# Optimization experiments

Measured on AMD Instinct MI355X. Metric: run time of the kernel, lower is better.

The kernel has to match this reference:

```python
import jax, jax.numpy as jnp
import numpy as np

HID = 128

def setup_inputs() -> dict:
    key = jax.random.key(0)
    ks = jax.random.split(key, 16)
    T, N, E = 32, 10000, 160000
    features = jax.random.normal(ks[0], (T, N, 1), dtype=jnp.float32)
    src = jax.random.randint(ks[1], (E,), 0, N)
    dst = jax.random.randint(ks[2], (E,), 0, N)
    s = 0.1
    # GraphConv params (stored as [in,out] so y = x @ W + b)
    W1 = jax.random.normal(ks[3], (1, 32), dtype=jnp.float32) * s
    b1 = jnp.zeros((32,), jnp.float32)
    W2 = jax.random.normal(ks[4], (32, HID), dtype=jnp.float32) * s
    b2 = jnp.zeros((HID,), jnp.float32)
    # attention-pool gate nn.Linear(128,1)
    gate_w = jax.random.normal(ks[5], (HID, 1), dtype=jnp.float32) * s
    gate_b = jnp.zeros((1,), jnp.float32)
    # GRU params, PyTorch layout: [3H, in], gate order (r, z, n)
    W_ih = jax.random.normal(ks[6], (3 * HID, HID), dtype=jnp.float32) * s
    W_hh = jax.random.normal(ks[7], (3 * HID, HID), dtype=jnp.float32) * s
    b_ih = jnp.zeros((3 * HID,), jnp.float32)
    b_hh = jnp.zeros((3 * HID,), jnp.float32)
    # dense layers ([in,out])
    d1_w = jax.random.normal(ks[8], (HID, 16), dtype=jnp.float32) * s
    d1_b = jnp.zeros((16,), jnp.float32)
    d2_w = jax.random.normal(ks[9], (16, 4), dtype=jnp.float32) * s
    d2_b = jnp.zeros((4,), jnp.float32)
    return {"features": features, "src": src, "dst": dst,
            "W1": W1, "b1": b1, "W2": W2, "b2": b2,
            "gate_w": gate_w, "gate_b": gate_b,
            "W_ih": W_ih, "W_hh": W_hh, "b_ih": b_ih, "b_hh": b_hh,
            "d1_w": d1_w, "d1_b": d1_b, "d2_w": d2_w, "d2_b": d2_b}


def reference(features, src, dst, W1, b1, W2, b2, gate_w, gate_b,
              W_ih, W_hh, b_ih, b_hh, d1_w, d1_b, d2_w, d2_b):
    T, N, _ = features.shape
    E = src.shape[0]
    ones = jnp.ones((E,), features.dtype)
    out_deg = jnp.clip(jax.ops.segment_sum(ones, src, num_segments=N), 1.0)
    in_deg = jnp.clip(jax.ops.segment_sum(ones, dst, num_segments=N), 1.0)
    norm_out = out_deg ** -0.5  # DGL GraphConv norm='both' (src side)
    norm_in = in_deg ** -0.5    # dst side

    def gconv(h, W, b):
        # h: [N, F] -> scale by src norm, gather, scatter-add to dst, scale, linear, SiLU
        msg = (h * norm_out[:, None])[src]               # [E, F]
        agg = jax.ops.segment_sum(msg, dst, num_segments=N)  # [N, F]
        return jax.nn.silu((agg * norm_in[:, None]) @ W + b)

    def per_frame(f):  # f: [N,1]
        return gconv(gconv(f, W1, b1), W2, b2)  # [N, HID]

    h = jax.vmap(per_frame)(features)  # [T, N, HID]

    # GlobalAttentionPooling: softmax over nodes of gate_nn(h)
    gate = h @ gate_w + gate_b                 # [T, N, 1]
    alpha = jax.nn.softmax(gate, axis=1)
    pooled = jnp.sum(alpha * h, axis=1)        # [T, HID]

    # single-layer GRU, batch=1, take final hidden state
    def gru_step(hprev, x):
        gi = x @ W_ih.T + b_ih
        gh = hprev @ W_hh.T + b_hh
        i_r, i_z, i_n = jnp.split(gi, 3)
        h_r, h_z, h_n = jnp.split(gh, 3)
        r = jax.nn.sigmoid(i_r + h_r)
        z = jax.nn.sigmoid(i_z + h_z)
        n = jnp.tanh(i_n + r * h_n)
        hnew = (1.0 - z) * n + z * hprev
        return hnew, None

    h0 = jnp.zeros((HID,), features.dtype)
    hT, _ = jax.lax.scan(gru_step, h0, pooled)

    out = jax.nn.silu(hT @ d1_w + d1_b)
    out = jax.nn.silu(out @ d2_w + d2_b)
    return jax.nn.sigmoid(out).reshape(1, 4)
```

## Files before the change

### kernel.cpp

```cpp
#include <hip/hip_runtime.h>
#include <stdint.h>

#define T_FRAMES 32
#define NNODES 10000
#define NEDGES 160000
#define HID 128
#define GXL 157

#define H1_SCALE 512.0f
#define H1_INV   (1.0f/512.0f)

typedef short v8s __attribute__((ext_vector_type(8)));
typedef float v4f __attribute__((ext_vector_type(4)));

static __device__ __forceinline__ ushort f2bf(float f){
  uint32_t u = __float_as_uint(f);
  u += 0x7FFFu + ((u >> 16) & 1u);
  return (ushort)(u >> 16);
}
static __device__ __forceinline__ float fsigm(float x){
  return __fdividef(1.0f, 1.0f + __expf(-x));
}
static __device__ __forceinline__ float fsilu(float x){
  return x * fsigm(x);
}
static __device__ __forceinline__ float ftanh(float x){
  return 2.0f * fsigm(2.0f * x) - 1.0f;
}


__global__ void k_degree(const int* __restrict__ src, const int* __restrict__ dst,
                         int* cnt_out, int* cnt_in, int E){
  int e = blockIdx.x*blockDim.x + threadIdx.x;
  if (e < E){
    atomicAdd(&cnt_out[src[e]], 1);
    atomicAdd(&cnt_in[dst[e]], 1);
  }
}

__global__ void __launch_bounds__(1024) k_scan(const int* __restrict__ cnt_in,
                                               const int* __restrict__ cnt_out,
                                               int* row_ptr, int* cursor,
                                               float* norm_out, float* norm_in, int N){
  __shared__ int wsum[16];
  __shared__ int carry_s, total_s;
  int tid = threadIdx.x;
  int lane = tid & 63, wid = tid >> 6;
  if (tid == 0) carry_s = 0;
  __syncthreads();
  for (int base = 0; base < N; base += 1024){
    int i = base + tid;
    int v = (i < N) ? cnt_in[i] : 0;
    if (i < N){
      norm_in[i]  = rsqrtf((float)max(v, 1));
      norm_out[i] = rsqrtf((float)max(cnt_out[i], 1));
    }
    int x = v;
    #pragma unroll
    for (int off = 1; off < 64; off <<= 1){
      int y = __shfl_up(x, off);
      if (lane >= off) x += y;
    }
    if (lane == 63) wsum[wid] = x;
    __syncthreads();
    if (tid == 0){
      int run = 0;
      #pragma unroll
      for (int w = 0; w < 16; ++w){ int tv = wsum[w]; wsum[w] = run; run += tv; }
      total_s = run;
    }
    __syncthreads();
    int excl = carry_s + wsum[wid] + x - v;
    if (i < N){ row_ptr[i] = excl; cursor[i] = excl; }
    __syncthreads();
    if (tid == 0) carry_s += total_s;
  }
  __syncthreads();
  if (tid == 0) row_ptr[N] = carry_s;
}

__global__ void k_fill(const int* __restrict__ src, const int* __restrict__ dst,
                       int* cursor, int* es, int E){
  int e = blockIdx.x*blockDim.x + threadIdx.x;
  if (e < E){
    int p = atomicAdd(&cursor[dst[e]], 1);
    es[p] = src[e];
  }
}


__global__ void __launch_bounds__(256) k_fnT(const float* __restrict__ feat,
                                             const float* __restrict__ norm_o,
                                             float* __restrict__ fnT, int N){
  __shared__ float sm[32][65];
  int n0 = blockIdx.x*64;
  int tid = threadIdx.x;
  for (int idx = tid; idx < 2048; idx += 256){
    int t = idx >> 6, i = idx & 63;
    int n = n0 + i;
    sm[t][i] = (n < N) ? feat[(size_t)t*N + n] : 0.f;
  }
  __syncthreads();
  for (int idx = tid; idx < 2048; idx += 256){
    int i = idx >> 5, t = idx & 31;
    int n = n0 + i;
    if (n < N) fnT[(size_t)n*32 + t] = sm[t][i] * norm_o[n];
  }
}


__global__ void __launch_bounds__(256) k_gconv1_nm(
    const float* __restrict__ fnT, const int* __restrict__ row_ptr,
    const int* __restrict__ es, const float* __restrict__ norm_in,
    const float* __restrict__ norm_out,
    const float* __restrict__ W1, const float* __restrict__ b1,
    uchar* __restrict__ h1s, int N){
  __shared__ float w1s[32], b1s[32];
  int tid = threadIdx.x;
  if (tid < 32){ w1s[tid] = W1[tid]; b1s[tid] = b1[tid]; }
  __syncthreads();
  int n = blockIdx.x*4 + (tid >> 6);
  int lane = tid & 63;
  int ep = lane >> 5, t = lane & 31;
  int s = row_ptr[n], d = row_ptr[n+1];
  float acc = 0.f;
  int e = s + ep;
  for (; e + 6 < d; e += 8){
    float v0 = fnT[(size_t)es[e]  *32 + t];
    float v1 = fnT[(size_t)es[e+2]*32 + t];
    float v2 = fnT[(size_t)es[e+4]*32 + t];
    float v3 = fnT[(size_t)es[e+6]*32 + t];
    acc += v0 + v1 + v2 + v3;
  }
  for (; e < d; e += 2)
    acc += fnT[(size_t)es[e]*32 + t];
  acc += __shfl_xor(acc, 32);
  float x1 = acc * norm_in[n];
  float x1p = __shfl(x1, lane >> 1);
  float no = norm_out[n];
  int j0 = (lane & 1) * 16;
  float hv[16];
  #pragma unroll
  for (int q = 0; q < 16; ++q)
    hv[q] = fsilu(fmaf(x1p, w1s[j0+q], b1s[j0+q])) * no;
  uint b[4] = {0u, 0u, 0u, 0u};
  #pragma unroll
  for (int q = 0; q < 16; ++q){
    float t8 = fminf(fmaxf(fmaf(hv[q], H1_SCALE, 128.5f), 0.f), 255.f);
    b[q >> 2] |= ((uint)(int)t8) << ((q & 3) * 8);
  }
  *(uint4*)(h1s + (size_t)n*1024 + lane*16) = make_uint4(b[0], b[1], b[2], b[3]);
}


__global__ void __launch_bounds__(256) k_gconv2_nm(
    const uchar* __restrict__ h1s, const int* __restrict__ row_ptr,
    const int* __restrict__ es, const float* __restrict__ norm_in,
    ushort* __restrict__ x2, int N){
  int tid = threadIdx.x;
  int n = blockIdx.x*4 + (tid >> 6);
  int lane = tid & 63;
  int s = row_ptr[n], d = row_ptr[n+1];
  float acc[16];
  #pragma unroll
  for (int i = 0; i < 16; ++i) acc[i] = 0.f;

  #define ACCB(v) do { \
    acc[0]  += (float)((v).x & 0xffu);         acc[1]  += (float)(((v).x >> 8) & 0xffu); \
    acc[2]  += (float)(((v).x >> 16) & 0xffu); acc[3]  += (float)((v).x >> 24); \
    acc[4]  += (float)((v).y & 0xffu);         acc[5]  += (float)(((v).y >> 8) & 0xffu); \
    acc[6]  += (float)(((v).y >> 16) & 0xffu); acc[7]  += (float)((v).y >> 24); \
    acc[8]  += (float)((v).z & 0xffu);         acc[9]  += (float)(((v).z >> 8) & 0xffu); \
    acc[10] += (float)(((v).z >> 16) & 0xffu); acc[11] += (float)((v).z >> 24); \
    acc[12] += (float)((v).w & 0xffu);         acc[13] += (float)(((v).w >> 8) & 0xffu); \
    acc[14] += (float)(((v).w >> 16) & 0xffu); acc[15] += (float)((v).w >> 24); \
  } while(0)

  int e = s;
  for (; e + 7 < d; e += 8){
    uint4 w0 = *((const uint4*)(h1s + (size_t)es[e]  *1024) + lane);
    uint4 w1 = *((const uint4*)(h1s + (size_t)es[e+1]*1024) + lane);
    uint4 w2 = *((const uint4*)(h1s + (size_t)es[e+2]*1024) + lane);
    uint4 w3 = *((const uint4*)(h1s + (size_t)es[e+3]*1024) + lane);
    uint4 w4 = *((const uint4*)(h1s + (size_t)es[e+4]*1024) + lane);
    uint4 w5 = *((const uint4*)(h1s + (size_t)es[e+5]*1024) + lane);
    uint4 w6 = *((const uint4*)(h1s + (size_t)es[e+6]*1024) + lane);
    uint4 w7 = *((const uint4*)(h1s + (size_t)es[e+7]*1024) + lane);
    ACCB(w0); ACCB(w1); ACCB(w2); ACCB(w3);
    ACCB(w4); ACCB(w5); ACCB(w6); ACCB(w7);
  }
  for (; e < d; ++e){
    uint4 w0 = *((const uint4*)(h1s + (size_t)es[e]*1024) + lane);
    ACCB(w0);
  }
  #undef ACCB

  float ni = norm_in[n];
  float corr = -128.0f * (float)(d - s);
  float sc = H1_INV * ni;
  uint w[8];
  #pragma unroll
  for (int q = 0; q < 8; ++q){
    float v0 = (acc[2*q]   + corr) * sc;
    float v1 = (acc[2*q+1] + corr) * sc;
    w[q] = (uint)f2bf(v0) | ((uint)f2bf(v1) << 16);
  }
  uint4* dp = (uint4*)(x2 + (size_t)n*1024 + lane*16);
  dp[0] = make_uint4(w[0], w[1], w[2], w[3]);
  dp[1] = make_uint4(w[4], w[5], w[6], w[7]);
}


__global__ void k_w2frag(const float* __restrict__ W2, ushort* __restrict__ W2F){
  int tid = blockIdx.x*blockDim.x + threadIdx.x;
  int j = tid & 7, l = (tid >> 3) & 63, i = tid >> 9;
  int g = l >> 4, n = l & 15;
  W2F[tid] = f2bf(W2[(g*8 + j)*128 + i*16 + n]);
}


__global__ void __launch_bounds__(256) k_linear_fused(
    const ushort* __restrict__ x2, const ushort* __restrict__ W2F,
    const float* __restrict__ b2, const float* __restrict__ gate_w,
    const float* __restrict__ gate_b,
    float* __restrict__ Zp, float* __restrict__ pooled_un, int N){
  __shared__ float pool_s[128];
  __shared__ float z_s[4];
  int t = blockIdx.y;
  int tid = threadIdx.x;
  int wave = tid >> 6, lane = tid & 63;
  int g = lane >> 4, n = lane & 15;
  if (tid < 128) pool_s[tid] = 0.f;
  if (tid < 4) z_s[tid] = 0.f;
  __syncthreads();
  int tile = blockIdx.x*4 + wave;
  bool active = (tile*16 < N);

  const v8s* W2Fv = (const v8s*)W2F;
  v8s bfrag[8];
  #pragma unroll
  for (int i = 0; i < 8; ++i) bfrag[i] = W2Fv[i*64 + lane];
  v4f acc[8];
  #pragma unroll
  for (int i = 0; i < 8; ++i){
    float bv = b2[i*16 + n];
    acc[i] = (v4f){bv, bv, bv, bv};
  }
  if (active){
    int nb = tile*16;
    const v8s* ap = (const v8s*)(x2 + (size_t)(nb + (lane & 15))*1024 + t*32);
    v8s a = ap[g];
    #pragma unroll
    for (int i = 0; i < 8; ++i)
      acc[i] = __builtin_amdgcn_mfma_f32_16x16x32_bf16(a, bfrag[i], acc[i], 0, 0, 0);

    float hs[8][4];
    #pragma unroll
    for (int i = 0; i < 8; ++i){
      #pragma unroll
      for (int r = 0; r < 4; ++r) hs[i][r] = fsilu(acc[i][r]);
    }
    float gw8[8];
    #pragma unroll
    for (int i = 0; i < 8; ++i) gw8[i] = gate_w[i*16 + n];
    float gp[4] = {0.f, 0.f, 0.f, 0.f};
    #pragma unroll
    for (int i = 0; i < 8; ++i){
      #pragma unroll
      for (int r = 0; r < 4; ++r) gp[r] += hs[i][r] * gw8[i];
    }
    #pragma unroll
    for (int m = 1; m < 16; m <<= 1){
      #pragma unroll
      for (int r = 0; r < 4; ++r) gp[r] += __shfl_xor(gp[r], m);
    }
    float gb = gate_b[0];
    float wn[4];
    #pragma unroll
    for (int r = 0; r < 4; ++r) wn[r] = __expf(gp[r] + gb);

    float se = (n == 0) ? (wn[0] + wn[1] + wn[2] + wn[3]) : 0.f;
    se += __shfl_xor(se, 16);
    se += __shfl_xor(se, 32);
    if (lane == 0) z_s[wave] = se;

    float cs[8];
    #pragma unroll
    for (int i = 0; i < 8; ++i){
      float c = 0.f;
      #pragma unroll
      for (int r = 0; r < 4; ++r) c += hs[i][r] * wn[r];
      c += __shfl_xor(c, 16);
      c += __shfl_xor(c, 32);
      cs[i] = c;
    }
    if (lane < 16){
      #pragma unroll
      for (int i = 0; i < 8; ++i) atomicAdd(&pool_s[i*16 + lane], cs[i]);
    }
  }
  __syncthreads();
  if (tid == 0)
    Zp[(size_t)t*GXL + blockIdx.x] = z_s[0] + z_s[1] + z_s[2] + z_s[3];
  if (tid < 128) atomicAdd(&pooled_un[(size_t)t*HID + tid], pool_s[tid]);
}


__global__ void __launch_bounds__(384) k_gi(const float* __restrict__ pooled_un,
                                            const float* __restrict__ Zp,
                                            const float* __restrict__ W_ih,
                                            const float* __restrict__ b_ih,
                                            float* __restrict__ gi_all){
  __shared__ float ps[HID];
  __shared__ float zred[6];
  int t = blockIdx.x, tid = threadIdx.x;
  int lane = tid & 63, wid = tid >> 6;
  float zs = 0.f;
  for (int i = tid; i < GXL; i += 384) zs += Zp[(size_t)t*GXL + i];
  #pragma unroll
  for (int m = 32; m; m >>= 1) zs += __shfl_xor(zs, m);
  if (lane == 0) zred[wid] = zs;
  __syncthreads();
  float invZ = __fdividef(1.0f, zred[0]+zred[1]+zred[2]+zred[3]+zred[4]+zred[5]);
  if (tid < HID) ps[tid] = pooled_un[(size_t)t*HID + tid] * invZ;
  __syncthreads();
  float acc = b_ih[tid];
  const float4* wr = (const float4*)(W_ih + (size_t)tid*HID);
  const float4* p4 = (const float4*)ps;
  #pragma unroll
  for (int q = 0; q < HID/4; ++q){
    float4 wv = wr[q], pv = p4[q];
    acc = fmaf(wv.x, pv.x, acc);
    acc = fmaf(wv.y, pv.y, acc);
    acc = fmaf(wv.z, pv.z, acc);
    acc = fmaf(wv.w, pv.w, acc);
  }
  gi_all[t*384 + tid] = acc;
}

__global__ void __launch_bounds__(768) k_gru(
    const float* __restrict__ gi_all, const float* __restrict__ W_hh,
    const float* __restrict__ b_hh,
    const float* __restrict__ d1_w, const float* __restrict__ d1_b,
    const float* __restrict__ d2_w, const float* __restrict__ d2_b,
    float* __restrict__ out){
  __shared__ float gi_s[T_FRAMES*3*HID];
  __shared__ float ps[2*384];
  __shared__ float h_s[HID];
  __shared__ float o1[16];
  int tid = threadIdx.x;
  int half = (tid >= 384) ? 1 : 0;
  int o = tid - half*384;

  for (int i = tid; i < T_FRAMES*3*HID; i += 768) gi_s[i] = gi_all[i];

  const float4* wr = (const float4*)(W_hh + (size_t)o*HID + half*64);
  #define LDW(i) float4 W##i = wr[i];
  LDW(0) LDW(1) LDW(2) LDW(3) LDW(4) LDW(5) LDW(6) LDW(7)
  LDW(8) LDW(9) LDW(10) LDW(11) LDW(12) LDW(13) LDW(14) LDW(15)
  #undef LDW
  float bh2 = half ? 0.f : b_hh[o];

  if (tid < HID) h_s[tid] = 0.f;
  __syncthreads();

  for (int t = 0; t < T_FRAMES; ++t){
    const float4* p4 = (const float4*)h_s + half*16;
    float acc = bh2;
    #define STEP(i) { float4 pv = p4[i]; \
      acc = fmaf(W##i.x, pv.x, acc); acc = fmaf(W##i.y, pv.y, acc); \
      acc = fmaf(W##i.z, pv.z, acc); acc = fmaf(W##i.w, pv.w, acc); }
    STEP(0) STEP(1) STEP(2) STEP(3) STEP(4) STEP(5) STEP(6) STEP(7)
    STEP(8) STEP(9) STEP(10) STEP(11) STEP(12) STEP(13) STEP(14) STEP(15)
    #undef STEP
    ps[tid] = acc;
    __syncthreads();
    if (tid < HID){
      const float* gi = gi_s + t*384;
      float ghr = ps[tid]       + ps[384+tid];
      float ghz = ps[128+tid]   + ps[512+tid];
      float ghn = ps[256+tid]   + ps[640+tid];
      float r  = fsigm(gi[tid]       + ghr);
      float z  = fsigm(gi[HID+tid]   + ghz);
      float nn = ftanh(gi[2*HID+tid] + r*ghn);
      h_s[tid] = (1.f - z)*nn + z*h_s[tid];
    }
    __syncthreads();
  }
  if (tid < 16){
    float acc = d1_b[tid];
    #pragma unroll 4
    for (int j = 0; j < HID; ++j) acc = fmaf(h_s[j], d1_w[j*16 + tid], acc);
    o1[tid] = fsilu(acc);
  }
  __syncthreads();
  if (tid < 4){
    float acc = d2_b[tid];
    #pragma unroll
    for (int j = 0; j < 16; ++j) acc = fmaf(o1[j], d2_w[j*4 + tid], acc);
    out[tid] = fsigm(fsilu(acc));
  }
}


extern "C" void kernel_launch(void* const* d_in, const int* in_sizes, int n_in,
                              void* d_out, int out_size, void* d_ws, size_t ws_size,
                              hipStream_t stream){
  const float* features = (const float*)d_in[0];
  const int*   src      = (const int*)  d_in[1];
  const int*   dst      = (const int*)  d_in[2];
  const float* W1       = (const float*)d_in[3];
  const float* b1       = (const float*)d_in[4];
  const float* W2       = (const float*)d_in[5];
  const float* b2       = (const float*)d_in[6];
  const float* gate_w   = (const float*)d_in[7];
  const float* gate_b   = (const float*)d_in[8];
  const float* W_ih     = (const float*)d_in[9];
  const float* W_hh     = (const float*)d_in[10];
  const float* b_ih     = (const float*)d_in[11];
  const float* b_hh     = (const float*)d_in[12];
  const float* d1_w     = (const float*)d_in[13];
  const float* d1_b     = (const float*)d_in[14];
  const float* d2_w     = (const float*)d_in[15];
  const float* d2_b     = (const float*)d_in[16];
  float* out = (float*)d_out;

  const int N = NNODES, E = NEDGES, T = T_FRAMES;

  char* base = (char*)d_ws;
  size_t off = 0;
  auto alloc = [&](size_t bytes)->void*{
    void* p = base + off;
    off = (off + bytes + 255) & ~(size_t)255;
    return p;
  };
  int*    cnt_out = (int*)   alloc((size_t)N*4);
  int*    cnt_in  = (int*)   alloc((size_t)N*4);
  float*  pooled  = (float*) alloc((size_t)T*HID*4);
  size_t zero_span = off;
  int*    row_ptr = (int*)   alloc((size_t)(N+1)*4);
  int*    cursor  = (int*)   alloc((size_t)N*4);
  float*  norm_o  = (float*) alloc((size_t)N*4);
  float*  norm_i  = (float*) alloc((size_t)N*4);
  int*    es      = (int*)   alloc((size_t)E*4);
  float*  fnT     = (float*) alloc((size_t)N*T*4);
  uchar*  h1s     = (uchar*) alloc((size_t)N*1024);
  ushort* x2      = (ushort*)alloc((size_t)N*T*32*2);
  float*  Zp      = (float*) alloc((size_t)T*GXL*4);
  float*  gi_all  = (float*) alloc((size_t)T*3*HID*4);
  ushort* W2F     = (ushort*)alloc((size_t)8*64*8*2);
  (void)ws_size; (void)in_sizes; (void)n_in; (void)out_size;

  hipMemsetAsync(d_ws, 0, zero_span, stream);

  k_degree<<<(E+255)/256, 256, 0, stream>>>(src, dst, cnt_out, cnt_in, E);
  k_scan  <<<1, 1024, 0, stream>>>(cnt_in, cnt_out, row_ptr, cursor, norm_o, norm_i, N);
  k_fill  <<<(E+255)/256, 256, 0, stream>>>(src, dst, cursor, es, E);

  k_fnT      <<<(N+63)/64, 256, 0, stream>>>(features, norm_o, fnT, N);
  k_gconv1_nm<<<N/4, 256, 0, stream>>>(fnT, row_ptr, es, norm_i, norm_o, W1, b1, h1s, N);
  k_gconv2_nm<<<N/4, 256, 0, stream>>>(h1s, row_ptr, es, norm_i, x2, N);

  k_w2frag<<<16, 256, 0, stream>>>(W2, W2F);

  k_linear_fused<<<dim3(GXL, T), 256, 0, stream>>>(x2, W2F, b2, gate_w, gate_b, Zp, pooled, N);

  k_gi <<<T, 384, 0, stream>>>(pooled, Zp, W_ih, b_ih, gi_all);
  k_gru<<<1, 768, 0, stream>>>(gi_all, W_hh, b_hh, d1_w, d1_b, d2_w, d2_b, out);
}
```

Measured before the change: 175.2 us.

## Single-pass scan, fold W2 fragment prep into fnT, two frames per linear block

```diff
diff --git a/kernel.cpp b/kernel.cpp
--- a/kernel.cpp
+++ b/kernel.cpp
@@ -43,40 +43,44 @@
                                                int* row_ptr, int* cursor,
                                                float* norm_out, float* norm_in, int N){
   __shared__ int wsum[16];
-  __shared__ int carry_s, total_s;
-  int tid = threadIdx.x;
-  int lane = tid & 63, wid = tid >> 6;
-  if (tid == 0) carry_s = 0;
-  __syncthreads();
-  for (int base = 0; base < N; base += 1024){
-    int i = base + tid;
-    int v = (i < N) ? cnt_in[i] : 0;
-    if (i < N){
-      norm_in[i]  = rsqrtf((float)max(v, 1));
-      norm_out[i] = rsqrtf((float)max(cnt_out[i], 1));
+  __shared__ int wexcl[16];
+  int tid = threadIdx.x, lane = tid & 63, wid = tid >> 6;
+  const int C = 10;
+  int base = tid * C;
+  int v[C];
+  int s = 0;
+  #pragma unroll
+  for (int i = 0; i < C; ++i){
+    int idx = base + i;
+    int c = (idx < N) ? cnt_in[idx] : 0;
+    v[i] = c;
+    s += c;
+    if (idx < N){
+      norm_in[idx]  = rsqrtf((float)max(c, 1));
+      norm_out[idx] = rsqrtf((float)max(cnt_out[idx], 1));
     }
-    int x = v;
+  }
+  int x = s;
+  #pragma unroll
+  for (int off = 1; off < 64; off <<= 1){
+    int y = __shfl_up(x, off);
+    if (lane >= off) x += y;
+  }
+  if (lane == 63) wsum[wid] = x;
+  __syncthreads();
+  if (tid == 0){
+    int run = 0;
     #pragma unroll
-    for (int off = 1; off < 64; off <<= 1){
-      int y = __shfl_up(x, off);
-      if (lane >= off) x += y;
-    }
-    if (lane == 63) wsum[wid] = x;
-    __syncthreads();
-    if (tid == 0){
-      int run = 0;
-      #pragma unroll
-      for (int w = 0; w < 16; ++w){ int tv = wsum[w]; wsum[w] = run; run += tv; }
-      total_s = run;
-    }
-    __syncthreads();
-    int excl = carry_s + wsum[wid] + x - v;
-    if (i < N){ row_ptr[i] = excl; cursor[i] = excl; }
-    __syncthreads();
-    if (tid == 0) carry_s += total_s;
-  }
-  __syncthreads();
-  if (tid == 0) row_ptr[N] = carry_s;
+    for (int w = 0; w < 16; ++w){ int t = wsum[w]; wexcl[w] = run; run += t; }
+    row_ptr[N] = run;
+  }
+  __syncthreads();
+  int run = wexcl[wid] + x - s;
+  #pragma unroll
+  for (int i = 0; i < C; ++i){
+    int idx = base + i;
+    if (idx < N){ row_ptr[idx] = run; cursor[idx] = run; run += v[i]; }
+  }
 }
 
 __global__ void k_fill(const int* __restrict__ src, const int* __restrict__ dst,
@@ -91,7 +95,9 @@
 
 __global__ void __launch_bounds__(256) k_fnT(const float* __restrict__ feat,
                                              const float* __restrict__ norm_o,
-                                             float* __restrict__ fnT, int N){
+                                             float* __restrict__ fnT,
+                                             const float* __restrict__ W2,
+                                             ushort* __restrict__ W2F, int N){
   __shared__ float sm[32][65];
   int n0 = blockIdx.x*64;
   int tid = threadIdx.x;
@@ -105,6 +111,12 @@
     int i = idx >> 5, t = idx & 31;
     int n = n0 + i;
     if (n < N) fnT[(size_t)n*32 + t] = sm[t][i] * norm_o[n];
+  }
+  if (blockIdx.x < 16){
+    int t2 = blockIdx.x*256 + tid;
+    int j = t2 & 7, l = (t2 >> 3) & 63, i = t2 >> 9;
+    int g = l >> 4, n = l & 15;
+    W2F[t2] = f2bf(W2[(g*8 + j)*128 + i*16 + n]);
   }
 }
 
@@ -211,27 +223,20 @@
 }
 
 
-__global__ void k_w2frag(const float* __restrict__ W2, ushort* __restrict__ W2F){
-  int tid = blockIdx.x*blockDim.x + threadIdx.x;
-  int j = tid & 7, l = (tid >> 3) & 63, i = tid >> 9;
-  int g = l >> 4, n = l & 15;
-  W2F[tid] = f2bf(W2[(g*8 + j)*128 + i*16 + n]);
-}
-
-
 __global__ void __launch_bounds__(256) k_linear_fused(
     const ushort* __restrict__ x2, const ushort* __restrict__ W2F,
     const float* __restrict__ b2, const float* __restrict__ gate_w,
     const float* __restrict__ gate_b,
     float* __restrict__ Zp, float* __restrict__ pooled_un, int N){
-  __shared__ float pool_s[128];
-  __shared__ float z_s[4];
-  int t = blockIdx.y;
+  __shared__ float pool_s[2][128];
+  __shared__ float z_s[2][4];
   int tid = threadIdx.x;
   int wave = tid >> 6, lane = tid & 63;
   int g = lane >> 4, n = lane & 15;
-  if (tid < 128) pool_s[tid] = 0.f;
-  if (tid < 4) z_s[tid] = 0.f;
+  int t0 = blockIdx.y * 2;
+  if (tid < 128) pool_s[0][tid] = 0.f;
+  else           pool_s[1][tid & 127] = 0.f;
+  if (tid < 8) z_s[tid >> 2][tid & 3] = 0.f;
   __syncthreads();
   int tile = blockIdx.x*4 + wave;
   bool active = (tile*16 < N);
@@ -240,69 +245,73 @@
   v8s bfrag[8];
   #pragma unroll
   for (int i = 0; i < 8; ++i) bfrag[i] = W2Fv[i*64 + lane];
-  v4f acc[8];
-  #pragma unroll
-  for (int i = 0; i < 8; ++i){
-    float bv = b2[i*16 + n];
-    acc[i] = (v4f){bv, bv, bv, bv};
-  }
+  float gw8[8], bv8[8];
+  #pragma unroll
+  for (int i = 0; i < 8; ++i){ gw8[i] = gate_w[i*16 + n]; bv8[i] = b2[i*16 + n]; }
+  float gb = gate_b[0];
+
   if (active){
     int nb = tile*16;
-    const v8s* ap = (const v8s*)(x2 + (size_t)(nb + (lane & 15))*1024 + t*32);
-    v8s a = ap[g];
-    #pragma unroll
-    for (int i = 0; i < 8; ++i)
-      acc[i] = __builtin_amdgcn_mfma_f32_16x16x32_bf16(a, bfrag[i], acc[i], 0, 0, 0);
-
-    float hs[8][4];
+    const ushort* xrow = x2 + (size_t)(nb + n)*1024 + g*8;
+    v8s a0 = *(const v8s*)(xrow + (size_t)t0*32);
+    v8s a1 = *(const v8s*)(xrow + (size_t)(t0+1)*32);
+    v4f acc0[8], acc1[8];
     #pragma unroll
     for (int i = 0; i < 8; ++i){
-      #pragma unroll
-      for (int r = 0; r < 4; ++r) hs[i][r] = fsilu(acc[i][r]);
+      acc0[i] = (v4f){bv8[i], bv8[i], bv8[i], bv8[i]};
+      acc1[i] = acc0[i];
     }
-    float gw8[8];
-    #pragma unroll
-    for (int i = 0; i < 8; ++i) gw8[i] = gate_w[i*16 + n];
-    float gp[4] = {0.f, 0.f, 0.f, 0.f};
     #pragma unroll
     for (int i = 0; i < 8; ++i){
-      #pragma unroll
-      for (int r = 0; r < 4; ++r) gp[r] += hs[i][r] * gw8[i];
+      acc0[i] = __builtin_amdgcn_mfma_f32_16x16x32_bf16(a0, bfrag[i], acc0[i], 0, 0, 0);
+      acc1[i] = __builtin_amdgcn_mfma_f32_16x16x32_bf16(a1, bfrag[i], acc1[i], 0, 0, 0);
     }
-    #pragma unroll
-    for (int m = 1; m < 16; m <<= 1){
-      #pragma unroll
-      for (int r = 0; r < 4; ++r) gp[r] += __shfl_xor(gp[r], m);
-    }
-    float gb = gate_b[0];
-    float wn[4];
-    #pragma unroll
-    for (int r = 0; r < 4; ++r) wn[r] = __expf(gp[r] + gb);
-
-    float se = (n == 0) ? (wn[0] + wn[1] + wn[2] + wn[3]) : 0.f;
-    se += __shfl_xor(se, 16);
-    se += __shfl_xor(se, 32);
-    if (lane == 0) z_s[wave] = se;
-
-    float cs[8];
-    #pragma unroll
-    for (int i = 0; i < 8; ++i){
-      float c = 0.f;
-      #pragma unroll
-      for (int r = 0; r < 4; ++r) c += hs[i][r] * wn[r];
-      c += __shfl_xor(c, 16);
-      c += __shfl_xor(c, 32);
-      cs[i] = c;
-    }
-    if (lane < 16){
-      #pragma unroll
-      for (int i = 0; i < 8; ++i) atomicAdd(&pool_s[i*16 + lane], cs[i]);
-    }
-  }
-  __syncthreads();
-  if (tid == 0)
-    Zp[(size_t)t*GXL + blockIdx.x] = z_s[0] + z_s[1] + z_s[2] + z_s[3];
-  if (tid < 128) atomicAdd(&pooled_un[(size_t)t*HID + tid], pool_s[tid]);
+
+    #define EPILOGUE(ACC, F) do { \
+      float hs[8][4]; \
+      _Pragma("unroll") \
+      for (int i = 0; i < 8; ++i){ \
+        _Pragma("unroll") \
+        for (int r = 0; r < 4; ++r) hs[i][r] = fsilu(ACC[i][r]); \
+      } \
+      float gp[4] = {0.f, 0.f, 0.f, 0.f}; \
+      _Pragma("unroll") \
+      for (int i = 0; i < 8; ++i){ \
+        _Pragma("unroll") \
+        for (int r = 0; r < 4; ++r) gp[r] += hs[i][r] * gw8[i]; \
+      } \
+      _Pragma("unroll") \
+      for (int m = 1; m < 16; m <<= 1){ \
+        _Pragma("unroll") \
+        for (int r = 0; r < 4; ++r) gp[r] += __shfl_xor(gp[r], m); \
+      } \
+      float wn[4]; \
+      _Pragma("unroll") \
+      for (int r = 0; r < 4; ++r) wn[r] = __expf(gp[r] + gb); \
+      float se = (n == 0) ? (wn[0]+wn[1]+wn[2]+wn[3]) : 0.f; \
+      se += __shfl_xor(se, 16); \
+      se += __shfl_xor(se, 32); \
+      if (lane == 0) z_s[F][wave] = se; \
+      _Pragma("unroll") \
+      for (int i = 0; i < 8; ++i){ \
+        float c = 0.f; \
+        _Pragma("unroll") \
+        for (int r = 0; r < 4; ++r) c += hs[i][r] * wn[r]; \
+        c += __shfl_xor(c, 16); \
+        c += __shfl_xor(c, 32); \
+        if (lane < 16) atomicAdd(&pool_s[F][i*16 + lane], c); \
+      } \
+    } while(0)
+
+    EPILOGUE(acc0, 0);
+    EPILOGUE(acc1, 1);
+    #undef EPILOGUE
+  }
+  __syncthreads();
+  if (tid < 2)
+    Zp[(size_t)(t0 + tid)*GXL + blockIdx.x] = z_s[tid][0]+z_s[tid][1]+z_s[tid][2]+z_s[tid][3];
+  { int f = tid >> 7, c = tid & 127;
+    atomicAdd(&pooled_un[(size_t)(t0 + f)*HID + c], pool_s[f][c]); }
 }
 
 
@@ -457,13 +466,11 @@
   k_scan  <<<1, 1024, 0, stream>>>(cnt_in, cnt_out, row_ptr, cursor, norm_o, norm_i, N);
   k_fill  <<<(E+255)/256, 256, 0, stream>>>(src, dst, cursor, es, E);
 
-  k_fnT      <<<(N+63)/64, 256, 0, stream>>>(features, norm_o, fnT, N);
+  k_fnT      <<<(N+63)/64, 256, 0, stream>>>(features, norm_o, fnT, W2, W2F, N);
   k_gconv1_nm<<<N/4, 256, 0, stream>>>(fnT, row_ptr, es, norm_i, norm_o, W1, b1, h1s, N);
   k_gconv2_nm<<<N/4, 256, 0, stream>>>(h1s, row_ptr, es, norm_i, x2, N);
 
-  k_w2frag<<<16, 256, 0, stream>>>(W2, W2F);
-
-  k_linear_fused<<<dim3(GXL, T), 256, 0, stream>>>(x2, W2F, b2, gate_w, gate_b, Zp, pooled, N);
+  k_linear_fused<<<dim3(GXL, T/2), 256, 0, stream>>>(x2, W2F, b2, gate_w, gate_b, Zp, pooled, N);
 
   k_gi <<<T, 384, 0, stream>>>(pooled, Zp, W_ih, b_ih, gi_all);
   k_gru<<<1, 768, 0, stream>>>(gi_all, W_hh, b_hh, d1_w, d1_b, d2_w, d2_b, out);
```

New measurement: 180.6 us. 1.03x slower.

## Single-pass scan, fold W2 fragment prep into fnT, frame-major x2 layout

Applied to the files above, without the earlier changes.

```diff
diff --git a/kernel.cpp b/kernel.cpp
--- a/kernel.cpp
+++ b/kernel.cpp
@@ -43,40 +43,44 @@
                                                int* row_ptr, int* cursor,
                                                float* norm_out, float* norm_in, int N){
   __shared__ int wsum[16];
-  __shared__ int carry_s, total_s;
-  int tid = threadIdx.x;
-  int lane = tid & 63, wid = tid >> 6;
-  if (tid == 0) carry_s = 0;
-  __syncthreads();
-  for (int base = 0; base < N; base += 1024){
-    int i = base + tid;
-    int v = (i < N) ? cnt_in[i] : 0;
-    if (i < N){
-      norm_in[i]  = rsqrtf((float)max(v, 1));
-      norm_out[i] = rsqrtf((float)max(cnt_out[i], 1));
-    }
-    int x = v;
-    #pragma unroll
-    for (int off = 1; off < 64; off <<= 1){
-      int y = __shfl_up(x, off);
-      if (lane >= off) x += y;
-    }
-    if (lane == 63) wsum[wid] = x;
-    __syncthreads();
-    if (tid == 0){
-      int run = 0;
-      #pragma unroll
-      for (int w = 0; w < 16; ++w){ int tv = wsum[w]; wsum[w] = run; run += tv; }
-      total_s = run;
-    }
-    __syncthreads();
-    int excl = carry_s + wsum[wid] + x - v;
-    if (i < N){ row_ptr[i] = excl; cursor[i] = excl; }
-    __syncthreads();
-    if (tid == 0) carry_s += total_s;
-  }
-  __syncthreads();
-  if (tid == 0) row_ptr[N] = carry_s;
+  __shared__ int wexcl[16];
+  int tid = threadIdx.x, lane = tid & 63, wid = tid >> 6;
+  const int C = 10;
+  int base = tid * C;
+  int v[C];
+  int s = 0;
+  #pragma unroll
+  for (int i = 0; i < C; ++i){
+    int idx = base + i;
+    int c = (idx < N) ? cnt_in[idx] : 0;
+    v[i] = c;
+    s += c;
+    if (idx < N){
+      norm_in[idx]  = rsqrtf((float)max(c, 1));
+      norm_out[idx] = rsqrtf((float)max(cnt_out[idx], 1));
+    }
+  }
+  int x = s;
+  #pragma unroll
+  for (int off = 1; off < 64; off <<= 1){
+    int y = __shfl_up(x, off);
+    if (lane >= off) x += y;
+  }
+  if (lane == 63) wsum[wid] = x;
+  __syncthreads();
+  if (tid == 0){
+    int run = 0;
+    #pragma unroll
+    for (int w = 0; w < 16; ++w){ int t = wsum[w]; wexcl[w] = run; run += t; }
+    row_ptr[N] = run;
+  }
+  __syncthreads();
+  int run = wexcl[wid] + x - s;
+  #pragma unroll
+  for (int i = 0; i < C; ++i){
+    int idx = base + i;
+    if (idx < N){ row_ptr[idx] = run; cursor[idx] = run; run += v[i]; }
+  }
 }
 
 __global__ void k_fill(const int* __restrict__ src, const int* __restrict__ dst,
@@ -91,7 +95,9 @@
 
 __global__ void __launch_bounds__(256) k_fnT(const float* __restrict__ feat,
                                              const float* __restrict__ norm_o,
-                                             float* __restrict__ fnT, int N){
+                                             float* __restrict__ fnT,
+                                             const float* __restrict__ W2,
+                                             ushort* __restrict__ W2F, int N){
   __shared__ float sm[32][65];
   int n0 = blockIdx.x*64;
   int tid = threadIdx.x;
@@ -105,6 +111,12 @@
     int i = idx >> 5, t = idx & 31;
     int n = n0 + i;
     if (n < N) fnT[(size_t)n*32 + t] = sm[t][i] * norm_o[n];
+  }
+  if (blockIdx.x < 16){
+    int t2 = blockIdx.x*256 + tid;
+    int j = t2 & 7, l = (t2 >> 3) & 63, i = t2 >> 9;
+    int g = l >> 4, n = l & 15;
+    W2F[t2] = f2bf(W2[(g*8 + j)*128 + i*16 + n]);
   }
 }
 
@@ -156,7 +168,7 @@
 __global__ void __launch_bounds__(256) k_gconv2_nm(
     const uchar* __restrict__ h1s, const int* __restrict__ row_ptr,
     const int* __restrict__ es, const float* __restrict__ norm_in,
-    ushort* __restrict__ x2, int N){
+    ushort* __restrict__ x2F, int N){
   int tid = threadIdx.x;
   int n = blockIdx.x*4 + (tid >> 6);
   int lane = tid & 63;
@@ -205,22 +217,14 @@
     float v1 = (acc[2*q+1] + corr) * sc;
     w[q] = (uint)f2bf(v0) | ((uint)f2bf(v1) << 16);
   }
-  uint4* dp = (uint4*)(x2 + (size_t)n*1024 + lane*16);
-  dp[0] = make_uint4(w[0], w[1], w[2], w[3]);
-  dp[1] = make_uint4(w[4], w[5], w[6], w[7]);
-}
-
-
-__global__ void k_w2frag(const float* __restrict__ W2, ushort* __restrict__ W2F){
-  int tid = blockIdx.x*blockDim.x + threadIdx.x;
-  int j = tid & 7, l = (tid >> 3) & 63, i = tid >> 9;
-  int g = l >> 4, n = l & 15;
-  W2F[tid] = f2bf(W2[(g*8 + j)*128 + i*16 + n]);
+  ushort* dp = x2F + (size_t)(lane >> 1)*N*32 + (size_t)n*32 + (lane & 1)*16;
+  *(uint4*)dp       = make_uint4(w[0], w[1], w[2], w[3]);
+  *((uint4*)dp + 1) = make_uint4(w[4], w[5], w[6], w[7]);
 }
 
 
 __global__ void __launch_bounds__(256) k_linear_fused(
-    const ushort* __restrict__ x2, const ushort* __restrict__ W2F,
+    const ushort* __restrict__ x2F, const ushort* __restrict__ W2F,
     const float* __restrict__ b2, const float* __restrict__ gate_w,
     const float* __restrict__ gate_b,
     float* __restrict__ Zp, float* __restrict__ pooled_un, int N){
@@ -248,8 +252,8 @@
   }
   if (active){
     int nb = tile*16;
-    const v8s* ap = (const v8s*)(x2 + (size_t)(nb + (lane & 15))*1024 + t*32);
-    v8s a = ap[g];
+    const v8s* ap = (const v8s*)(x2F + (size_t)t*N*32 + (size_t)nb*32);
+    v8s a = ap[n*4 + g];
     #pragma unroll
     for (int i = 0; i < 8; ++i)
       acc[i] = __builtin_amdgcn_mfma_f32_16x16x32_bf16(a, bfrag[i], acc[i], 0, 0, 0);
@@ -445,7 +449,7 @@
   int*    es      = (int*)   alloc((size_t)E*4);
   float*  fnT     = (float*) alloc((size_t)N*T*4);
   uchar*  h1s     = (uchar*) alloc((size_t)N*1024);
-  ushort* x2      = (ushort*)alloc((size_t)N*T*32*2);
+  ushort* x2F     = (ushort*)alloc((size_t)T*N*32*2);
   float*  Zp      = (float*) alloc((size_t)T*GXL*4);
   float*  gi_all  = (float*) alloc((size_t)T*3*HID*4);
   ushort* W2F     = (ushort*)alloc((size_t)8*64*8*2);
@@ -457,13 +461,11 @@
   k_scan  <<<1, 1024, 0, stream>>>(cnt_in, cnt_out, row_ptr, cursor, norm_o, norm_i, N);
   k_fill  <<<(E+255)/256, 256, 0, stream>>>(src, dst, cursor, es, E);
 
-  k_fnT      <<<(N+63)/64, 256, 0, stream>>>(features, norm_o, fnT, N);
+  k_fnT      <<<(N+63)/64, 256, 0, stream>>>(features, norm_o, fnT, W2, W2F, N);
   k_gconv1_nm<<<N/4, 256, 0, stream>>>(fnT, row_ptr, es, norm_i, norm_o, W1, b1, h1s, N);
-  k_gconv2_nm<<<N/4, 256, 0, stream>>>(h1s, row_ptr, es, norm_i, x2, N);
-
-  k_w2frag<<<16, 256, 0, stream>>>(W2, W2F);
-
-  k_linear_fused<<<dim3(GXL, T), 256, 0, stream>>>(x2, W2F, b2, gate_w, gate_b, Zp, pooled, N);
+  k_gconv2_nm<<<N/4, 256, 0, stream>>>(h1s, row_ptr, es, norm_i, x2F, N);
+
+  k_linear_fused<<<dim3(GXL, T), 256, 0, stream>>>(x2F, W2F, b2, gate_w, gate_b, Zp, pooled, N);
 
   k_gi <<<T, 384, 0, stream>>>(pooled, Zp, W_ih, b_ih, gi_all);
   k_gru<<<1, 768, 0, stream>>>(gi_all, W_hh, b_hh, d1_w, d1_b, d2_w, d2_b, out);
```

Result: no change. 178.4 us, median of 2 (+1.8%).
